# Optimization experiments

Hardware: AMD Instinct MI355X
Metric: run time of the kernel (lower is better)

The kernel has to match this reference:

```python
import jax, jax.numpy as jnp
import numpy as np

INIT_TAU = 2.0     # init_tau
V_TH = 1.0         # v_threshold
V_RESET = 0.0      # v_reset
SG_SLOPE = 10.0    # fast-sigmoid surrogate slope
IN_SZ = 8192
OUT_SZ = 8192


def setup_inputs() -> dict:
    key = jax.random.key(0)
    k1, k2, k3, k4 = jax.random.split(key, 4)
    x = jax.random.normal(k1, (IN_SZ,), jnp.float32)
    u = jax.random.normal(k2, (OUT_SZ,), jnp.float32)
    # eligibility trace dL-free state, same shape as the dense kernel
    J_u_W = jax.random.normal(k3, (IN_SZ, OUT_SZ), jnp.float32) * 0.01
    W = jax.random.normal(k4, (IN_SZ, OUT_SZ), jnp.float32) * (1.0 / np.sqrt(IN_SZ))
    return {"x": x, "u": u, "J_u_W": J_u_W, "W": W}


def reference(x, u, J_u_W, W):
    """One OSTL step (the f_fwd path: cell update + eligibility-trace update).

    Cell (SpikingBlockMod with dense connection + LIF dynamics):
      I      = x @ W
      u_new  = sigmoid(init_tau) * u + I
      s      = H(u_new - v_th)               (heaviside spike)
      u_out  = u_new - stop_grad(s) * (v_th - v_reset)   (detached soft reset)

    Trace update (per-parameter, here only the kernel W):
      grad_u_u = sig_tau (diagonal), grad_u_W = x[:, None]
      J_u_W'   = sig_tau * J_u_W + x[:, None]
    """
    sig_tau = jax.nn.sigmoid(jnp.asarray(INIT_TAU, x.dtype))
    I = x @ W                                  # [out]
    u_new = sig_tau * u + I                    # [out]
    v = u_new - V_TH
    s = (v > 0).astype(x.dtype)                # [out] spikes
    u_out = u_new - s * (V_TH - V_RESET)       # detached reset
    J_u_W_new = sig_tau * J_u_W + x[:, None]   # [in, out] eligibility trace
    return (u_out, J_u_W_new, s)
```

## Files before the change

### kernel.cpp

```cpp
#include <hip/hip_runtime.h>

#define IN_SZ 8192
#define OUT_SZ 8192

#define SIG_TAU 0.8807970779778823f

__global__ void zeroI_kernel(float* __restrict__ I) {
    int j = blockIdx.x * blockDim.x + threadIdx.x;
    if (j < OUT_SZ) I[j] = 0.0f;
}

template <int ROWS>
__global__ void gemv_partial_kernel(const float* __restrict__ x,
                                    const float* __restrict__ W,
                                    float* __restrict__ Iacc) {
    __shared__ float xs[ROWS];
    const int tid  = threadIdx.x;
    const int col0 = blockIdx.x * 1024 + tid * 4;
    const int row0 = blockIdx.y * ROWS;

    if (tid < ROWS) xs[tid] = x[row0 + tid];
    __syncthreads();

    float4 acc = make_float4(0.f, 0.f, 0.f, 0.f);
    const float* wp = W + (size_t)row0 * OUT_SZ + col0;
#pragma unroll 8
    for (int r = 0; r < ROWS; ++r) {
        float4 w = *(const float4*)wp;
        float xi = xs[r];
        acc.x += xi * w.x;
        acc.y += xi * w.y;
        acc.z += xi * w.z;
        acc.w += xi * w.w;
        wp += OUT_SZ;
    }
    atomicAdd(&Iacc[col0 + 0], acc.x);
    atomicAdd(&Iacc[col0 + 1], acc.y);
    atomicAdd(&Iacc[col0 + 2], acc.z);
    atomicAdd(&Iacc[col0 + 3], acc.w);
}

__global__ void finalize_kernel(const float* __restrict__ u,
                                float* __restrict__ out) {
    int j = blockIdx.x * blockDim.x + threadIdx.x;
    if (j >= OUT_SZ) return;
    float I     = out[j];
    float u_new = SIG_TAU * u[j] + I;
    float s     = (u_new - 1.0f > 0.0f) ? 1.0f : 0.0f;
    out[j] = u_new - s;
    out[(size_t)OUT_SZ + (size_t)IN_SZ * OUT_SZ + j] = s;
}

__global__ void jup_kernel(const float* __restrict__ x,
                           const float* __restrict__ J,
                           float* __restrict__ Jout) {
    const int row = blockIdx.x;
    const float xi = x[row];
    const float4* jp = (const float4*)(J + (size_t)row * OUT_SZ);
    float4* op = (float4*)(Jout + (size_t)row * OUT_SZ);
    const int tid = threadIdx.x;
#pragma unroll
    for (int c = 0; c < OUT_SZ / 4 / 256; ++c) {
        float4 v = jp[c * 256 + tid];
        v.x = SIG_TAU * v.x + xi;
        v.y = SIG_TAU * v.y + xi;
        v.z = SIG_TAU * v.z + xi;
        v.w = SIG_TAU * v.w + xi;
        op[c * 256 + tid] = v;
    }
}

extern "C" void kernel_launch(void* const* d_in, const int* in_sizes, int n_in,
                              void* d_out, int out_size, void* d_ws, size_t ws_size,
                              hipStream_t stream) {
    const float* x = (const float*)d_in[0];
    const float* u = (const float*)d_in[1];
    const float* J = (const float*)d_in[2];
    const float* W = (const float*)d_in[3];
    float* out = (float*)d_out;

    jup_kernel<<<IN_SZ, 256, 0, stream>>>(x, J, out + OUT_SZ);

    zeroI_kernel<<<(OUT_SZ + 255) / 256, 256, 0, stream>>>(out);
    gemv_partial_kernel<64><<<dim3(OUT_SZ / 1024, IN_SZ / 64), 256, 0, stream>>>(x, W, out);
    finalize_kernel<<<(OUT_SZ + 255) / 256, 256, 0, stream>>>(u, out);
}
```

Measured before the change: 609.6 us.

## Fuse trace update into GEMV pass and replace atomics with partial-sum reduction

Merges the eligibility-trace update into the GEMV kernel so W and J rows are streamed by the same blocks in one launch. Replaces atomicAdd accumulation into the output with per-row-chunk partial sums in workspace, reduced in the finalize kernel. This removes the zeroing kernel, two launches and atomic contention, at the cost of a 4MB partial buffer and a longer reduction loop in finalize.

Result: no change. 616.6 us (+1.2%).

```diff
diff --git a/kernel.cpp b/kernel.cpp
--- a/kernel.cpp
+++ b/kernel.cpp
@@ -5,69 +5,67 @@
 
 #define SIG_TAU 0.8807970779778823f
 
-__global__ void zeroI_kernel(float* __restrict__ I) {
-    int j = blockIdx.x * blockDim.x + threadIdx.x;
-    if (j < OUT_SZ) I[j] = 0.0f;
-}
+#define ROWS 64
+#define COLS_PER_BLOCK 1024
+#define NUM_RC (IN_SZ / ROWS)
+#define NUM_CT (OUT_SZ / COLS_PER_BLOCK)
 
-template <int ROWS>
-__global__ void gemv_partial_kernel(const float* __restrict__ x,
-                                    const float* __restrict__ W,
-                                    float* __restrict__ Iacc) {
+__global__ void fused_kernel(const float* __restrict__ x,
+                             const float* __restrict__ J,
+                             const float* __restrict__ W,
+                             float* __restrict__ Jout,
+                             float* __restrict__ partial) {
     __shared__ float xs[ROWS];
     const int tid  = threadIdx.x;
-    const int col0 = blockIdx.x * 1024 + tid * 4;
-    const int row0 = blockIdx.y * ROWS;
+    const int ct   = blockIdx.x;
+    const int rc   = blockIdx.y;
+    const int col0 = ct * COLS_PER_BLOCK + tid * 4;
+    const int row0 = rc * ROWS;
 
     if (tid < ROWS) xs[tid] = x[row0 + tid];
     __syncthreads();
 
+    const size_t base = (size_t)row0 * OUT_SZ + col0;
+    const float* wp = W + base;
+    const float* jp = J + base;
+    float*       op = Jout + base;
+
     float4 acc = make_float4(0.f, 0.f, 0.f, 0.f);
-    const float* wp = W + (size_t)row0 * OUT_SZ + col0;
 #pragma unroll 8
     for (int r = 0; r < ROWS; ++r) {
+        const float xi = xs[r];
         float4 w = *(const float4*)wp;
-        float xi = xs[r];
+        float4 j = *(const float4*)jp;
         acc.x += xi * w.x;
         acc.y += xi * w.y;
         acc.z += xi * w.z;
         acc.w += xi * w.w;
+        float4 o;
+        o.x = SIG_TAU * j.x + xi;
+        o.y = SIG_TAU * j.y + xi;
+        o.z = SIG_TAU * j.z + xi;
+        o.w = SIG_TAU * j.w + xi;
+        *(float4*)op = o;
         wp += OUT_SZ;
+        jp += OUT_SZ;
+        op += OUT_SZ;
     }
-    atomicAdd(&Iacc[col0 + 0], acc.x);
-    atomicAdd(&Iacc[col0 + 1], acc.y);
-    atomicAdd(&Iacc[col0 + 2], acc.z);
-    atomicAdd(&Iacc[col0 + 3], acc.w);
+    *(float4*)(partial + (size_t)rc * OUT_SZ + col0) = acc;
 }
 
 __global__ void finalize_kernel(const float* __restrict__ u,
+                                const float* __restrict__ partial,
                                 float* __restrict__ out) {
-    int j = blockIdx.x * blockDim.x + threadIdx.x;
+    const int j = blockIdx.x * blockDim.x + threadIdx.x;
     if (j >= OUT_SZ) return;
-    float I     = out[j];
+    float I = 0.f;
+#pragma unroll 8
+    for (int rc = 0; rc < NUM_RC; ++rc)
+        I += partial[(size_t)rc * OUT_SZ + j];
     float u_new = SIG_TAU * u[j] + I;
-    float s     = (u_new - 1.0f > 0.0f) ? 1.0f : 0.0f;
+    float s     = (u_new > 1.0f) ? 1.0f : 0.0f;
     out[j] = u_new - s;
     out[(size_t)OUT_SZ + (size_t)IN_SZ * OUT_SZ + j] = s;
-}
-
-__global__ void jup_kernel(const float* __restrict__ x,
-                           const float* __restrict__ J,
-                           float* __restrict__ Jout) {
-    const int row = blockIdx.x;
-    const float xi = x[row];
-    const float4* jp = (const float4*)(J + (size_t)row * OUT_SZ);
-    float4* op = (float4*)(Jout + (size_t)row * OUT_SZ);
-    const int tid = threadIdx.x;
-#pragma unroll
-    for (int c = 0; c < OUT_SZ / 4 / 256; ++c) {
-        float4 v = jp[c * 256 + tid];
-        v.x = SIG_TAU * v.x + xi;
-        v.y = SIG_TAU * v.y + xi;
-        v.z = SIG_TAU * v.z + xi;
-        v.w = SIG_TAU * v.w + xi;
-        op[c * 256 + tid] = v;
-    }
 }
 
 extern "C" void kernel_launch(void* const* d_in, const int* in_sizes, int n_in,
@@ -77,11 +75,9 @@
     const float* u = (const float*)d_in[1];
     const float* J = (const float*)d_in[2];
     const float* W = (const float*)d_in[3];
-    float* out = (float*)d_out;
+    float* out     = (float*)d_out;
+    float* partial = (float*)d_ws;
 
-    jup_kernel<<<IN_SZ, 256, 0, stream>>>(x, J, out + OUT_SZ);
-
-    zeroI_kernel<<<(OUT_SZ + 255) / 256, 256, 0, stream>>>(out);
-    gemv_partial_kernel<64><<<dim3(OUT_SZ / 1024, IN_SZ / 64), 256, 0, stream>>>(x, W, out);
-    finalize_kernel<<<(OUT_SZ + 255) / 256, 256, 0, stream>>>(u, out);
+    fused_kernel<<<dim3(NUM_CT, NUM_RC), 256, 0, stream>>>(x, J, W, out + OUT_SZ, partial);
+    finalize_kernel<<<(OUT_SZ + 255) / 256, 256, 0, stream>>>(u, partial, out);
 }
```
